# Performance work log

Measured on AMD Instinct MI355X. Metric: run time of the kernel, lower is better.

## Reference

```python
import jax, jax.numpy as jnp
import numpy as np

N = 100000      # num nodes
E = 1600000     # num edges
B = 256         # num graphs in batch
D_IN = 128
H = 256
BN_EPS = 1e-5


def setup_inputs() -> dict:
    key = jax.random.key(0)
    ks = jax.random.split(key, 16)
    inp = {}
    inp["x"] = jax.random.normal(ks[0], (N, D_IN), jnp.float32)
    inp["edge_index"] = jax.random.randint(ks[1], (2, E), 0, N, jnp.int32)
    inp["edge_weight"] = jax.random.uniform(ks[2], (E,), jnp.float32)
    inp["batch"] = jnp.sort(jax.random.randint(ks[3], (N,), 0, B, jnp.int32))
    # GCN layer 1
    inp["W1"] = jax.random.normal(ks[4], (D_IN, H), jnp.float32) * 0.05
    inp["b1"] = jnp.zeros((H,), jnp.float32)
    inp["g1"] = jnp.ones((H,), jnp.float32)
    inp["be1"] = jnp.zeros((H,), jnp.float32)
    inp["rm1"] = jnp.zeros((H,), jnp.float32)
    inp["rv1"] = jnp.ones((H,), jnp.float32)
    # GCN layer 2
    inp["W2"] = jax.random.normal(ks[5], (H, H), jnp.float32) * 0.05
    inp["b2"] = jnp.zeros((H,), jnp.float32)
    inp["g2"] = jnp.ones((H,), jnp.float32)
    inp["be2"] = jnp.zeros((H,), jnp.float32)
    inp["rm2"] = jnp.zeros((H,), jnp.float32)
    inp["rv2"] = jnp.ones((H,), jnp.float32)
    # classifier: Linear(256,256)+BN, Linear(256,128)+BN, Linear(128,2)
    inp["cW1"] = jax.random.normal(ks[6], (H, 256), jnp.float32) * 0.05
    inp["cb1"] = jnp.zeros((256,), jnp.float32)
    inp["cg1"] = jnp.ones((256,), jnp.float32)
    inp["cbe1"] = jnp.zeros((256,), jnp.float32)
    inp["crm1"] = jnp.zeros((256,), jnp.float32)
    inp["crv1"] = jnp.ones((256,), jnp.float32)
    inp["cW2"] = jax.random.normal(ks[7], (256, 128), jnp.float32) * 0.05
    inp["cb2"] = jnp.zeros((128,), jnp.float32)
    inp["cg2"] = jnp.ones((128,), jnp.float32)
    inp["cbe2"] = jnp.zeros((128,), jnp.float32)
    inp["crm2"] = jnp.zeros((128,), jnp.float32)
    inp["crv2"] = jnp.ones((128,), jnp.float32)
    inp["cW3"] = jax.random.normal(ks[8], (128, 2), jnp.float32) * 0.05
    inp["cb3"] = jnp.zeros((2,), jnp.float32)
    return inp


def _bn(x, g, b, rm, rv):
    # eval-mode BatchNorm1d with running stats
    return (x - rm) * jax.lax.rsqrt(rv + BN_EPS) * g + b


def _gcn_conv(x, W, b, src, dst, ew):
    # PyG GCNConv: add self-loops (weight 1), symmetric normalization
    deg = jax.ops.segment_sum(ew, dst, num_segments=N) + 1.0  # incl. self loop
    dinv = jnp.where(deg > 0, jax.lax.rsqrt(deg), 0.0)        # [N]
    h = x @ W                                                  # [N, out]
    norm = dinv[src] * ew * dinv[dst]                          # [E]
    agg = jax.ops.segment_sum(h[src] * norm[:, None], dst, num_segments=N)
    agg = agg + h * (dinv * dinv)[:, None]                     # self-loop term
    return agg + b


def _forward(x, edge_index, edge_weight, batch,
             W1, b1, g1, be1, rm1, rv1,
             W2, b2, g2, be2, rm2, rv2,
             cW1, cb1, cg1, cbe1, crm1, crv1,
             cW2, cb2, cg2, cbe2, crm2, crv2,
             cW3, cb3):
    src, dst = edge_index[0], edge_index[1]
    # layer 0 (no residual: i == 0)
    h = jax.nn.relu(_bn(_gcn_conv(x, W1, b1, src, dst, edge_weight), g1, be1, rm1, rv1))
    res = h
    # layer 1 (residual: dims match, i > 0); dropout = identity (eval)
    h = jax.nn.relu(_bn(_gcn_conv(h, W2, b2, src, dst, edge_weight), g2, be2, rm2, rv2))
    h = h + res
    # global mean pool per graph
    cnt = jax.ops.segment_sum(jnp.ones((N,), x.dtype), batch, num_segments=B)
    emb = jax.ops.segment_sum(h, batch, num_segments=B) / jnp.maximum(cnt, 1.0)[:, None]
    # classifier MLP
    z = jax.nn.relu(_bn(emb @ cW1 + cb1, cg1, cbe1, crm1, crv1))
    z = jax.nn.relu(_bn(z @ cW2 + cb2, cg2, cbe2, crm2, crv2))
    logits = z @ cW3 + cb3
    return logits, emb


def reference(x, edge_index, edge_weight, batch,
              W1, b1, g1, be1, rm1, rv1,
              W2, b2, g2, be2, rm2, rv2,
              cW1, cb1, cg1, cbe1, crm1, crv1,
              cW2, cb2, cg2, cbe2, crm2, crv2,
              cW3, cb3):
    return _forward(x, edge_index, edge_weight, batch,
                    W1, b1, g1, be1, rm1, rv1,
                    W2, b2, g2, be2, rm2, rv2,
                    cW1, cb1, cg1, cbe1, crm1, crv1,
                    cW2, cb2, cg2, cbe2, crm2, crv2,
                    cW3, cb3)
```

## Files before the change

kernel.cpp:

```cpp
#include <hip/hip_runtime.h>
#include <stdint.h>

#define NN 100000
#define NE 1600000
#define NB 256
#define DIN 128
#define HH 256
#define BN_EPS 1e-5f

typedef unsigned short bf16_t;
typedef __attribute__((ext_vector_type(8))) short short8;
typedef __attribute__((ext_vector_type(4))) short short4v;
typedef __attribute__((ext_vector_type(4))) float f32x4;
typedef __attribute__((ext_vector_type(2))) float f32x2;

struct __align__(8) EPair { int c; float v; };

#define DEG_MASK ((1ULL << 40) - 1ULL)
#define DEG_ONE  (1ULL << 40)
#define FXS 1048576.0f

__device__ __forceinline__ float bf2f(unsigned short u) {
    union { unsigned int i; float f; } v;
    v.i = ((unsigned int)u) << 16;
    return v.f;
}
__device__ __forceinline__ bf16_t f2bf(float f) {
    union { float f; unsigned int i; } v;
    v.f = f;
    unsigned int x = v.i;
    return (bf16_t)((x + 0x7fffu + ((x >> 16) & 1u)) >> 16);
}
__device__ __forceinline__ float ldp(const void* b, int i, int f) {
    return f ? ((const float*)b)[i] : bf2f(((const unsigned short*)b)[i]);
}
__device__ __forceinline__ int dflag_from(const void* rv) {
    return ((((const unsigned int*)rv)[0] & 0xffffu) == 0u) ? 1 : 0;
}

__device__ __forceinline__ void fmadd_row8p(f32x2* acc2, uint2 w, float v) {
#if defined(__HIP_DEVICE_COMPILE__)
    f32x2 vv = {v, v};
    acc2[0] += __builtin_amdgcn_cvt_pk_f32_fp8((int)w.x, false) * vv;
    acc2[1] += __builtin_amdgcn_cvt_pk_f32_fp8((int)w.x, true)  * vv;
    acc2[2] += __builtin_amdgcn_cvt_pk_f32_fp8((int)w.y, false) * vv;
    acc2[3] += __builtin_amdgcn_cvt_pk_f32_fp8((int)w.y, true)  * vv;
#else
    (void)acc2; (void)w; (void)v;
#endif
}
__device__ __forceinline__ unsigned char enc_fp8(float v) {
#if defined(__HIP_DEVICE_COMPILE__)
    int pk = __builtin_amdgcn_cvt_pk_fp8_f32(v, v, 0, false);
    return (unsigned char)(pk & 0xff);
#else
    (void)v; return 0;
#endif
}
__device__ __forceinline__ unsigned int pack4_fp8(float a, float b, float c, float d) {
#if defined(__HIP_DEVICE_COMPILE__)
    int w = __builtin_amdgcn_cvt_pk_fp8_f32(a, b, 0, false);
    w = __builtin_amdgcn_cvt_pk_fp8_f32(c, d, w, true);
    return (unsigned int)w;
#else
    (void)a; (void)b; (void)c; (void)d; return 0;
#endif
}

__device__ __forceinline__ void pack_one(const void* __restrict__ W, bf16_t* __restrict__ P,
                                         int S, int idx, int f) {
    int lane = idx & 63;
    int ts = idx >> 6;
    int s = ts % S;
    int t = ts / S;
    int q = lane >> 4, m = lane & 15;
    int colbase = t * 16 + m;
    int krow = 32 * s + 8 * q;
#pragma unroll
    for (int j = 0; j < 8; j++) P[idx * 8 + j] = f2bf(ldp(W, (krow + j) * 256 + colbase, f));
}

__global__ __launch_bounds__(256) void prep_kernel(const void* __restrict__ x, unsigned int* __restrict__ xc8,
                                                   const void* __restrict__ ew,
                                                   const int* __restrict__ dst,
                                                   const int* __restrict__ batch,
                                                   unsigned long long* __restrict__ cd8,
                                                   unsigned char* __restrict__ occ,
                                                   int* __restrict__ gcount,
                                                   const void* __restrict__ W1, bf16_t* __restrict__ P1,
                                                   const void* __restrict__ W2, bf16_t* __restrict__ P2,
                                                   const void* __restrict__ rv) {
    int i = blockIdx.x * blockDim.x + threadIdx.x;
    int stride = gridDim.x * blockDim.x;
    int shard = blockIdx.x & 7;
    int f = dflag_from(rv);
    if (i < 12288) {
        if (i < 4096) pack_one(W1, P1, 4, i, f);
        else          pack_one(W2, P2, 8, i - 4096, f);
    }
    if (f) {
        const float4* xs = (const float4*)x;
        for (int j = i; j < NN * DIN / 4; j += stride) {
            float4 w = xs[j];
            xc8[j] = pack4_fp8(w.x, w.y, w.z, w.w);
        }
    } else {
        const uint2* xs = (const uint2*)x;
        for (int j = i; j < NN * DIN / 4; j += stride) {
            uint2 w = xs[j];
            xc8[j] = pack4_fp8(bf2f((unsigned short)(w.x & 0xffffu)), bf2f((unsigned short)(w.x >> 16)),
                               bf2f((unsigned short)(w.y & 0xffffu)), bf2f((unsigned short)(w.y >> 16)));
        }
    }
    for (int j = i; j < NE; j += stride) {
        float w = ldp(ew, j, f);
        int d = dst[j];
        unsigned long long wfx = (unsigned long long)(unsigned int)(w * FXS + 0.5f);
        unsigned long long old = atomicAdd(&cd8[(size_t)shard * NN + d], DEG_ONE | wfx);
        occ[j] = (unsigned char)(old >> 40);
    }
    int lane = threadIdx.x & 63;
    for (int j = i; j < NN; j += stride) {
        int b = batch[j];
        bool boundary = (lane == 0) || (j == 0) || (batch[j - 1] != b);
        unsigned long long bmask = __ballot(boundary);
        bool islast = (lane == 63) || (j + 1 >= NN) || (batch[j + 1] != b);
        if (islast) {
            unsigned long long below = bmask & ((lane == 63) ? ~0ull : ((1ull << (lane + 1)) - 1ull));
            int first = 63 - __builtin_clzll(below);
            atomicAdd(&gcount[b], lane - first + 1);
        }
    }
}

#define SCAN_NB ((NN + 1023) / 1024)

__global__ __launch_bounds__(1024) void scanA(const unsigned long long* __restrict__ cd8,
                                              int* __restrict__ rowptr,
                                              float* __restrict__ dinv,
                                              int* __restrict__ bsum) {
    __shared__ int wsum[16];
    int tid = threadIdx.x, lane = tid & 63, wid = tid >> 6;
    int i = blockIdx.x * 1024 + tid;
    int v = 0;
    if (i < NN) {
        float wf = 0.f;
#pragma unroll
        for (int k = 0; k < 8; k++) {
            unsigned long long cv = cd8[(size_t)k * NN + i];
            v += (int)(cv >> 40);
            wf += (float)(cv & DEG_MASK);
        }
        dinv[i] = rsqrtf(wf * (1.0f / FXS) + 1.0f);
    }
    int sc = v;
#pragma unroll
    for (int off = 1; off < 64; off <<= 1) {
        int t = __shfl_up(sc, off, 64);
        if (lane >= off) sc += t;
    }
    if (lane == 63) wsum[wid] = sc;
    __syncthreads();
    if (wid == 0 && lane < 16) {
        int ws = wsum[lane];
        int scw = ws;
#pragma unroll
        for (int off = 1; off < 16; off <<= 1) {
            int t = __shfl_up(scw, off, 64);
            if (lane >= off) scw += t;
        }
        if (lane == 15) bsum[blockIdx.x] = scw;
        wsum[lane] = scw - ws;
    }
    __syncthreads();
    if (i < NN) rowptr[i] = wsum[wid] + sc - v;
}

__global__ __launch_bounds__(64) void scanB(int* __restrict__ bsum, int* __restrict__ rowptr,
                                            const int* __restrict__ gcount, int* __restrict__ gptr) {
    int lane = threadIdx.x;
    {
        int i0 = lane * 2;
        int v0 = (i0 < SCAN_NB) ? bsum[i0] : 0;
        int v1 = (i0 + 1 < SCAN_NB) ? bsum[i0 + 1] : 0;
        int tsum = v0 + v1;
        int sc = tsum;
#pragma unroll
        for (int off = 1; off < 64; off <<= 1) {
            int t = __shfl_up(sc, off, 64);
            if (lane >= off) sc += t;
        }
        int excl = sc - tsum;
        if (i0 < SCAN_NB) bsum[i0] = excl;
        if (i0 + 1 < SCAN_NB) bsum[i0 + 1] = excl + v0;
        if (lane == 63) rowptr[NN] = sc;
    }
    {
        int i0 = lane * 4;
        int v0 = gcount[i0], v1 = gcount[i0 + 1], v2 = gcount[i0 + 2], v3 = gcount[i0 + 3];
        int tsum = v0 + v1 + v2 + v3;
        int sc = tsum;
#pragma unroll
        for (int off = 1; off < 64; off <<= 1) {
            int t = __shfl_up(sc, off, 64);
            if (lane >= off) sc += t;
        }
        int excl = sc - tsum;
        gptr[i0] = excl;
        gptr[i0 + 1] = excl + v0;
        gptr[i0 + 2] = excl + v0 + v1;
        gptr[i0 + 3] = excl + v0 + v1 + v2;
        if (lane == 63) gptr[256] = sc;
    }
}

__global__ __launch_bounds__(1024) void scanC(int* __restrict__ rowptr, const int* __restrict__ bsum,
                                              const unsigned long long* __restrict__ cd8,
                                              int* __restrict__ offs) {
    int i = blockIdx.x * 1024 + threadIdx.x;
    if (i < NN) {
        int rp = rowptr[i] + bsum[blockIdx.x];
        rowptr[i] = rp;
        int cum = rp;
#pragma unroll
        for (int k = 0; k < 8; k++) {
            offs[(size_t)k * NN + i] = cum;
            cum += (int)(cd8[(size_t)k * NN + i] >> 40);
        }
    }
}

__global__ __launch_bounds__(256) void scatter_kernel(const int* __restrict__ src,
                                                      const int* __restrict__ dst,
                                                      const void* __restrict__ ew,
                                                      const float* __restrict__ dinv,
                                                      const int* __restrict__ offs,
                                                      const unsigned char* __restrict__ occ,
                                                      EPair* __restrict__ ep,
                                                      const void* __restrict__ rv) {
    int i = blockIdx.x * blockDim.x + threadIdx.x;
    int f = dflag_from(rv);
    int shard = blockIdx.x & 7;
    if (i < NE) {
        int s = src[i], d = dst[i];
        float nv = dinv[s] * ldp(ew, i, f) * dinv[d];
        int pos = offs[(size_t)shard * NN + d] + occ[i];
        EPair pr;
        pr.c = s;
        pr.v = nv;
        ep[pos] = pr;
    }
}

template <int K, bool WRITE_OUT, bool ACCUM>
__global__ __launch_bounds__(256, 6) void fused_layer(
        const void* __restrict__ Xv,
        const bf16_t* __restrict__ P,
        const int* __restrict__ rowptr,
        const EPair* __restrict__ ep,
        const float* __restrict__ dinv,
        const int* __restrict__ batch,
        const void* __restrict__ bias,
        const void* __restrict__ gam,
        const void* __restrict__ bet,
        const void* __restrict__ rmean,
        const void* __restrict__ rvar,
        void* __restrict__ outbuf,
        float* __restrict__ partial,
        float* __restrict__ partial2,
        float* __restrict__ embf) {
    constexpr int S = K / 32;
    constexpr int ROWELL = K + 8;
    constexpr int LPR = K / 8;
    constexpr int EDG = 64 / LPR;
    constexpr int UN = 8;
    constexpr int BE = EDG * UN;
    __shared__ __align__(16) bf16_t T[16 * ROWELL];
    const char* Xb = (const char*)Xv;
    int fl = dflag_from(rvar);
    int widx = threadIdx.x >> 6;
    int lane = threadIdx.x & 63;
    int h = lane / LPR;
    int l = lane % LPR;
    int f0 = l * 8;
    int rowbase = blockIdx.x * 16;

    int rp = rowptr[rowbase + (lane < 17 ? lane : 16)];
    float dvv = dinv[rowbase + (lane < 16 ? lane : 15)];

    int j0 = widx * 4;
    EPair win = ep[__shfl(rp, j0) + lane];
    for (int j = 0; j < 4; j++) {
        int r = j0 + j;
        int e0 = __shfl(rp, r);
        int e1 = __shfl(rp, r + 1);
        int n = e1 - e0;
        float di = __shfl(dvv, r);
        int node = rowbase + r;
        EPair nxtwin = ep[e1 + lane];
        f32x2 acc2[4];
#pragma unroll
        for (int c = 0; c < 4; c++) acc2[c] = (f32x2){0.f, 0.f};
        EPair cw = win;
        uint2 wself = *(const uint2*)(Xb + (size_t)node * K + l * 8);
        if (n <= 2 * BE) {
            uint2 wregA[UN], wregB[UN];
            float vregA[UN], vregB[UN];
#pragma unroll
            for (int u = 0; u < UN; u++) {
                int idx = EDG * u + h;
                bool ok = idx < n;
                int sl = ok ? idx : 0;
                int c = __shfl(cw.c, sl);
                float v = __shfl(cw.v, sl);
                wregA[u] = *(const uint2*)(Xb + (size_t)(ok ? c : node) * K + l * 8);
                vregA[u] = ok ? v : 0.f;
            }
#pragma unroll
            for (int u = 0; u < UN; u++) {
                int idx = BE + EDG * u + h;
                bool ok = idx < n;
                int sl = ok ? idx : 0;
                int c = __shfl(cw.c, sl);
                float v = __shfl(cw.v, sl);
                wregB[u] = *(const uint2*)(Xb + (size_t)(ok ? c : node) * K + l * 8);
                vregB[u] = ok ? v : 0.f;
            }
#pragma unroll
            for (int u = 0; u < UN; u++) fmadd_row8p(acc2, wregA[u], vregA[u]);
#pragma unroll
            for (int u = 0; u < UN; u++) fmadd_row8p(acc2, wregB[u], vregB[u]);
        } else {
            int base = 0;
            while (base < n) {
                int winend = n - base;
                if (winend > 64) winend = 64;
                for (int s0 = 0; s0 < winend; s0 += BE) {
                    uint2 wreg[UN];
                    float vreg[UN];
#pragma unroll
                    for (int u = 0; u < UN; u++) {
                        int idx = s0 + EDG * u + h;
                        bool ok = idx < winend;
                        int sl = ok ? idx : 0;
                        int c = __shfl(cw.c, sl);
                        float v = __shfl(cw.v, sl);
                        wreg[u] = *(const uint2*)(Xb + (size_t)(ok ? c : node) * K + l * 8);
                        vreg[u] = ok ? v : 0.f;
                    }
#pragma unroll
                    for (int u = 0; u < UN; u++) fmadd_row8p(acc2, wreg[u], vreg[u]);
                }
                base += winend;
                if (base < n) cw = ep[e0 + base + lane];
            }
        }
        fmadd_row8p(acc2, wself, (h == 0) ? di * di : 0.f);
        float acc[8];
#pragma unroll
        for (int c = 0; c < 4; c++) { acc[2 * c] = acc2[c][0]; acc[2 * c + 1] = acc2[c][1]; }
#pragma unroll
        for (int d = LPR; d < 64; d <<= 1) {
#pragma unroll
            for (int c = 0; c < 8; c++) acc[c] += __shfl_xor(acc[c], d);
        }
        if (h == 0) {
            short8 o;
#pragma unroll
            for (int c = 0; c < 8; c++) o[c] = (short)f2bf(acc[c]);
            *(short8*)&T[r * ROWELL + f0] = o;
        }
        win = nxtwin;
    }
    __syncthreads();

    int m = lane & 15, q = lane >> 4;
    f32x4 acc16[4];
#pragma unroll
    for (int tt = 0; tt < 4; tt++) acc16[tt] = (f32x4){0.f, 0.f, 0.f, 0.f};
#pragma unroll
    for (int s = 0; s < S; s++) {
        short8 af = *(const short8*)&T[m * ROWELL + 32 * s + 8 * q];
#pragma unroll
        for (int tt = 0; tt < 4; tt++) {
            int t = j0 + tt;
            short8 bfr = *(const short8*)(P + ((size_t)(t * S + s) * 64 + lane) * 8);
            acc16[tt] = __builtin_amdgcn_mfma_f32_16x16x32_bf16(af, bfr, acc16[tt], 0, 0, 0);
        }
    }
    if (WRITE_OUT) __syncthreads();
    unsigned char* T8 = (unsigned char*)T;

    int g0 = batch[rowbase];
    int g15 = batch[rowbase + 15];
    int rg[4];
#pragma unroll
    for (int r = 0; r < 4; r++) rg[r] = batch[rowbase + q * 4 + r];
#pragma unroll
    for (int tt = 0; tt < 4; tt++) {
        int col = (j0 + tt) * 16 + m;
        float a = rsqrtf(ldp(rvar, col, fl) + BN_EPS) * ldp(gam, col, fl);
        float bc = (ldp(bias, col, fl) - ldp(rmean, col, fl)) * a + ldp(bet, col, fl);
        float cs0 = 0.f, cs1 = 0.f;
#pragma unroll
        for (int r = 0; r < 4; r++) {
            int row = q * 4 + r;
            float v = fmaxf(acc16[tt][r] * a + bc, 0.f);
            if (WRITE_OUT) T8[row * 256 + col] = enc_fp8(v);
            if (rg[r] == g0) cs0 += v;
            else if (rg[r] == g15) cs1 += v;
            else atomicAdd(&embf[(size_t)rg[r] * 256 + col], v);
        }
        cs0 += __shfl_xor(cs0, 16, 64);
        cs0 += __shfl_xor(cs0, 32, 64);
        cs1 += __shfl_xor(cs1, 16, 64);
        cs1 += __shfl_xor(cs1, 32, 64);
        if (q == 0) {
            size_t pidx = (size_t)blockIdx.x * 256 + col;
            partial[pidx]  = (ACCUM ? partial[pidx]  : 0.f) + cs0;
            partial2[pidx] = (ACCUM ? partial2[pidx] : 0.f) + cs1;
        }
    }
    if (WRITE_OUT) {
        __syncthreads();
        int tid = threadIdx.x;
        uint4 wv = *(const uint4*)&T8[tid * 16];
        *(uint4*)((char*)outbuf + (size_t)rowbase * 256 + tid * 16) = wv;
    }
}

__global__ __launch_bounds__(256) void classifier_kernel(const float* __restrict__ partial,
                                                         const float* __restrict__ partial2,
                                                         const int* __restrict__ gptr,
                                                         const float* __restrict__ embf,
                                                         const void* cW1, const void* cb1,
                                                         const void* cg1, const void* cbe1,
                                                         const void* crm1, const void* crv1,
                                                         const void* cW2, const void* cb2,
                                                         const void* cg2, const void* cbe2,
                                                         const void* crm2, const void* crv2,
                                                         const void* cW3, const void* cb3,
                                                         void* __restrict__ d_out) {
    int g = blockIdx.x, tid = threadIdx.x;
    int fl = dflag_from(crv1);
    __shared__ float se[256];
    __shared__ float z1[256];
    __shared__ float z2[128];
    int s = gptr[g], e = gptr[g + 1];
    float acc = embf[g * 256 + tid];
    int blo = (s + 15) >> 4, bhi = (e + 15) >> 4;
    for (int b = blo; b < bhi; b++) acc += partial[(size_t)b * 256 + tid];
    int bs = s >> 4;
    if ((s & 15) && (16 * bs + 15) < e) acc += partial2[(size_t)bs * 256 + tid];
    float mval = acc / fmaxf((float)(e - s), 1.f);
    se[tid] = mval;
    if (fl) ((float*)d_out)[512 + g * 256 + tid] = mval;
    else    ((bf16_t*)d_out)[512 + g * 256 + tid] = f2bf(mval);
    __syncthreads();
    {
        float sm = 0.f;
#pragma unroll 8
        for (int k = 0; k < 256; k++) sm += se[k] * ldp(cW1, k * 256 + tid, fl);
        sm += ldp(cb1, tid, fl);
        sm = (sm - ldp(crm1, tid, fl)) * rsqrtf(ldp(crv1, tid, fl) + BN_EPS) * ldp(cg1, tid, fl) + ldp(cbe1, tid, fl);
        z1[tid] = fmaxf(sm, 0.f);
    }
    __syncthreads();
    if (tid < 128) {
        float sm = 0.f;
#pragma unroll 8
        for (int k = 0; k < 256; k++) sm += z1[k] * ldp(cW2, k * 128 + tid, fl);
        sm += ldp(cb2, tid, fl);
        sm = (sm - ldp(crm2, tid, fl)) * rsqrtf(ldp(crv2, tid, fl) + BN_EPS) * ldp(cg2, tid, fl) + ldp(cbe2, tid, fl);
        z2[tid] = fmaxf(sm, 0.f);
    }
    __syncthreads();
    if (tid < 2) {
        float sm = 0.f;
        for (int k = 0; k < 128; k++) sm += z2[k] * ldp(cW3, k * 2 + tid, fl);
        sm += ldp(cb3, tid, fl);
        if (fl) ((float*)d_out)[g * 2 + tid] = sm;
        else    ((bf16_t*)d_out)[g * 2 + tid] = f2bf(sm);
    }
}

extern "C" void kernel_launch(void* const* d_in, const int* in_sizes, int n_in,
                              void* d_out, int out_size, void* d_ws, size_t ws_size,
                              hipStream_t stream) {
    const void* x    = d_in[0];
    const int*  eidx = (const int*)d_in[1];
    const void* ew   = d_in[2];
    const int*  batch= (const int*)d_in[3];
    const void* W1   = d_in[4];
    const void* b1   = d_in[5];
    const void* g1   = d_in[6];
    const void* be1  = d_in[7];
    const void* rm1  = d_in[8];
    const void* rv1  = d_in[9];
    const void* W2   = d_in[10];
    const void* b2   = d_in[11];
    const void* g2   = d_in[12];
    const void* be2  = d_in[13];
    const void* rm2  = d_in[14];
    const void* rv2  = d_in[15];
    const void* cW1  = d_in[16];
    const void* cb1  = d_in[17];
    const void* cg1  = d_in[18];
    const void* cbe1 = d_in[19];
    const void* crm1 = d_in[20];
    const void* crv1 = d_in[21];
    const void* cW2  = d_in[22];
    const void* cb2  = d_in[23];
    const void* cg2  = d_in[24];
    const void* cbe2 = d_in[25];
    const void* crm2 = d_in[26];
    const void* crv2 = d_in[27];
    const void* cW3  = d_in[28];
    const void* cb3  = d_in[29];

    const int* src = eidx;
    const int* dst = eidx + NE;

    char* p = (char*)d_ws;
    auto alloc = [&](size_t bytes) -> void* {
        void* r = (void*)p;
        p += (bytes + 255) & ~(size_t)255;
        return r;
    };
    unsigned long long* cd8 = (unsigned long long*)alloc((size_t)8 * NN * 8);
    int*    gcount = (int*)alloc((size_t)NB * 4);
    float*  embf   = (float*)alloc((size_t)NB * 256 * 4);
    size_t zspan = (char*)p - (char*)cd8;
    int*    rowptr = (int*)alloc((size_t)(NN + 1) * 4);
    float*  dinv   = (float*)alloc((size_t)NN * 4);
    int*    bsum   = (int*)alloc((size_t)SCAN_NB * 4);
    int*    gptr   = (int*)alloc((size_t)(NB + 1) * 4);
    int*    offs   = (int*)alloc((size_t)8 * NN * 4);
    unsigned char* occ = (unsigned char*)alloc((size_t)NE);
    float*  partial = (float*)alloc((size_t)(NN / 16) * 256 * 4);
    float*  partial2= (float*)alloc((size_t)(NN / 16) * 256 * 4);
    EPair*  ep     = (EPair*)alloc((size_t)(NE + 64) * 8);
    unsigned int* xc8 = (unsigned int*)alloc((size_t)NN * DIN);
    bf16_t* pW1    = (bf16_t*)alloc((size_t)DIN * 256 * 2);
    bf16_t* pW2    = (bf16_t*)alloc((size_t)256 * 256 * 2);
    void*   hl     = alloc((size_t)NN * 256);

    (void)hipMemsetAsync(cd8, 0, zspan, stream);

    prep_kernel<<<2048, 256, 0, stream>>>(x, xc8, ew, dst, batch, cd8, occ, gcount,
                                          W1, pW1, W2, pW2, rv1);
    scanA<<<SCAN_NB, 1024, 0, stream>>>(cd8, rowptr, dinv, bsum);
    scanB<<<1, 64, 0, stream>>>(bsum, rowptr, gcount, gptr);
    scanC<<<SCAN_NB, 1024, 0, stream>>>(rowptr, bsum, cd8, offs);
    scatter_kernel<<<NE / 256, 256, 0, stream>>>(src, dst, ew, dinv, offs, occ, ep, rv1);

    int blocks = NN / 16;
    fused_layer<128, true, false><<<blocks, 256, 0, stream>>>(
        xc8, pW1, rowptr, ep, dinv, batch, b1, g1, be1, rm1, rv1, hl, partial, partial2, embf);
    fused_layer<256, false, true><<<blocks, 256, 0, stream>>>(
        hl, pW2, rowptr, ep, dinv, batch, b2, g2, be2, rm2, rv2, nullptr, partial, partial2, embf);

    classifier_kernel<<<NB, 256, 0, stream>>>(partial, partial2, gptr, embf,
                                              cW1, cb1, cg1, cbe1, crm1, crv1,
                                              cW2, cb2, cg2, cbe2, crm2, crv2,
                                              cW3, cb3, d_out);
}
```

Before: 527.0 us.

## Merge three scan kernels into one with grid barrier; vectorize edge scatter

Replaces the three-kernel prefix scan (block scan, single-block scan, fixup) with one kernel. The last-arriving block computes the block prefixes and graph pointers, and the other blocks spin on a flag, which removes two launches and the re-read of the per-shard counts. The edge scatter now handles four edges per thread with vector loads of src, dst and occupancy bytes. The shuffle-index select in the aggregation loop is also dropped. The spin barrier relies on all blocks being co-resident, which is a deadlock risk if they are not.

Result: no change. 531.3 us (+0.8%).

```diff
diff --git a/kernel.cpp b/kernel.cpp
--- a/kernel.cpp
+++ b/kernel.cpp
@@ -135,23 +135,34 @@
 
 #define SCAN_NB ((NN + 1023) / 1024)
 
-__global__ __launch_bounds__(1024) void scanA(const unsigned long long* __restrict__ cd8,
-                                              int* __restrict__ rowptr,
-                                              float* __restrict__ dinv,
-                                              int* __restrict__ bsum) {
+__global__ __launch_bounds__(1024) void scan_all(const unsigned long long* __restrict__ cd8,
+                                                 const int* __restrict__ gcount,
+                                                 int* __restrict__ rowptr,
+                                                 float* __restrict__ dinv,
+                                                 int* __restrict__ offs,
+                                                 int* __restrict__ gptr,
+                                                 int* __restrict__ ctrl,
+                                                 int* __restrict__ partials,
+                                                 int* __restrict__ prefix) {
     __shared__ int wsum[16];
+    __shared__ int s_off;
     int tid = threadIdx.x, lane = tid & 63, wid = tid >> 6;
-    int i = blockIdx.x * 1024 + tid;
+    int b = blockIdx.x;
+    int i = b * 1024 + tid;
     int v = 0;
+    int shardcnt[8];
+    float wf = 0.f;
     if (i < NN) {
-        float wf = 0.f;
 #pragma unroll
         for (int k = 0; k < 8; k++) {
             unsigned long long cv = cd8[(size_t)k * NN + i];
-            v += (int)(cv >> 40);
+            shardcnt[k] = (int)(cv >> 40);
+            v += shardcnt[k];
             wf += (float)(cv & DEG_MASK);
         }
-        dinv[i] = rsqrtf(wf * (1.0f / FXS) + 1.0f);
+    } else {
+#pragma unroll
+        for (int k = 0; k < 8; k++) shardcnt[k] = 0;
     }
     int sc = v;
 #pragma unroll
@@ -169,63 +180,45 @@
             int t = __shfl_up(scw, off, 64);
             if (lane >= off) scw += t;
         }
-        if (lane == 15) bsum[blockIdx.x] = scw;
+        if (lane == 15 && tid == 15) {}
         wsum[lane] = scw - ws;
-    }
-    __syncthreads();
-    if (i < NN) rowptr[i] = wsum[wid] + sc - v;
-}
-
-__global__ __launch_bounds__(64) void scanB(int* __restrict__ bsum, int* __restrict__ rowptr,
-                                            const int* __restrict__ gcount, int* __restrict__ gptr) {
-    int lane = threadIdx.x;
-    {
-        int i0 = lane * 2;
-        int v0 = (i0 < SCAN_NB) ? bsum[i0] : 0;
-        int v1 = (i0 + 1 < SCAN_NB) ? bsum[i0 + 1] : 0;
-        int tsum = v0 + v1;
-        int sc = tsum;
-#pragma unroll
-        for (int off = 1; off < 64; off <<= 1) {
-            int t = __shfl_up(sc, off, 64);
-            if (lane >= off) sc += t;
-        }
-        int excl = sc - tsum;
-        if (i0 < SCAN_NB) bsum[i0] = excl;
-        if (i0 + 1 < SCAN_NB) bsum[i0 + 1] = excl + v0;
-        if (lane == 63) rowptr[NN] = sc;
-    }
-    {
-        int i0 = lane * 4;
-        int v0 = gcount[i0], v1 = gcount[i0 + 1], v2 = gcount[i0 + 2], v3 = gcount[i0 + 3];
-        int tsum = v0 + v1 + v2 + v3;
-        int sc = tsum;
-#pragma unroll
-        for (int off = 1; off < 64; off <<= 1) {
-            int t = __shfl_up(sc, off, 64);
-            if (lane >= off) sc += t;
-        }
-        int excl = sc - tsum;
-        gptr[i0] = excl;
-        gptr[i0 + 1] = excl + v0;
-        gptr[i0 + 2] = excl + v0 + v1;
-        gptr[i0 + 3] = excl + v0 + v1 + v2;
-        if (lane == 63) gptr[256] = sc;
-    }
-}
-
-__global__ __launch_bounds__(1024) void scanC(int* __restrict__ rowptr, const int* __restrict__ bsum,
-                                              const unsigned long long* __restrict__ cd8,
-                                              int* __restrict__ offs) {
-    int i = blockIdx.x * 1024 + threadIdx.x;
+        if (lane == 15) partials[b] = scw;
+    }
+    __syncthreads();
+    if (tid == 0) {
+        __threadfence();
+        int old = atomicAdd(&ctrl[0], 1);
+        if (old == SCAN_NB - 1) {
+            __threadfence();
+            int run = 0;
+            for (int p = 0; p < SCAN_NB; p++) {
+                prefix[p] = run;
+                run += partials[p];
+            }
+            rowptr[NN] = run;
+            int g = 0;
+            for (int p = 0; p < NB; p++) {
+                gptr[p] = g;
+                g += gcount[p];
+            }
+            gptr[NB] = g;
+            __threadfence();
+            atomicExch(&ctrl[1], 1);
+        }
+        while (atomicAdd(&ctrl[1], 0) == 0) {}
+        __threadfence();
+        s_off = prefix[b];
+    }
+    __syncthreads();
     if (i < NN) {
-        int rp = rowptr[i] + bsum[blockIdx.x];
-        rowptr[i] = rp;
-        int cum = rp;
+        int base = s_off + wsum[wid] + (sc - v);
+        rowptr[i] = base;
+        dinv[i] = rsqrtf(wf * (1.0f / FXS) + 1.0f);
+        int cum = base;
 #pragma unroll
         for (int k = 0; k < 8; k++) {
             offs[(size_t)k * NN + i] = cum;
-            cum += (int)(cd8[(size_t)k * NN + i] >> 40);
+            cum += shardcnt[k];
         }
     }
 }
@@ -238,15 +231,22 @@
                                                       const unsigned char* __restrict__ occ,
                                                       EPair* __restrict__ ep,
                                                       const void* __restrict__ rv) {
-    int i = blockIdx.x * blockDim.x + threadIdx.x;
+    int t = blockIdx.x * blockDim.x + threadIdx.x;
+    if (t >= NE / 4) return;
     int f = dflag_from(rv);
-    int shard = blockIdx.x & 7;
-    if (i < NE) {
-        int s = src[i], d = dst[i];
-        float nv = dinv[s] * ldp(ew, i, f) * dinv[d];
-        int pos = offs[(size_t)shard * NN + d] + occ[i];
+    int base = t * 4;
+    int shard = (base >> 8) & 7;
+    uint4 s4 = ((const uint4*)src)[t];
+    uint4 d4 = ((const uint4*)dst)[t];
+    uint oc4 = ((const unsigned int*)occ)[t];
+    int ss[4] = {(int)s4.x, (int)s4.y, (int)s4.z, (int)s4.w};
+    int dd[4] = {(int)d4.x, (int)d4.y, (int)d4.z, (int)d4.w};
+#pragma unroll
+    for (int k = 0; k < 4; k++) {
+        float nv = dinv[ss[k]] * ldp(ew, base + k, f) * dinv[dd[k]];
+        int pos = offs[(size_t)shard * NN + dd[k]] + (int)((oc4 >> (8 * k)) & 0xffu);
         EPair pr;
-        pr.c = s;
+        pr.c = ss[k];
         pr.v = nv;
         ep[pos] = pr;
     }
@@ -310,9 +310,8 @@
             for (int u = 0; u < UN; u++) {
                 int idx = EDG * u + h;
                 bool ok = idx < n;
-                int sl = ok ? idx : 0;
-                int c = __shfl(cw.c, sl);
-                float v = __shfl(cw.v, sl);
+                int c = __shfl(cw.c, idx);
+                float v = __shfl(cw.v, idx);
                 wregA[u] = *(const uint2*)(Xb + (size_t)(ok ? c : node) * K + l * 8);
                 vregA[u] = ok ? v : 0.f;
             }
@@ -320,9 +319,8 @@
             for (int u = 0; u < UN; u++) {
                 int idx = BE + EDG * u + h;
                 bool ok = idx < n;
-                int sl = ok ? idx : 0;
-                int c = __shfl(cw.c, sl);
-                float v = __shfl(cw.v, sl);
+                int c = __shfl(cw.c, idx);
+                float v = __shfl(cw.v, idx);
                 wregB[u] = *(const uint2*)(Xb + (size_t)(ok ? c : node) * K + l * 8);
                 vregB[u] = ok ? v : 0.f;
             }
@@ -342,9 +340,8 @@
                     for (int u = 0; u < UN; u++) {
                         int idx = s0 + EDG * u + h;
                         bool ok = idx < winend;
-                        int sl = ok ? idx : 0;
-                        int c = __shfl(cw.c, sl);
-                        float v = __shfl(cw.v, sl);
+                        int c = __shfl(cw.c, idx);
+                        float v = __shfl(cw.v, idx);
                         wreg[u] = *(const uint2*)(Xb + (size_t)(ok ? c : node) * K + l * 8);
                         vreg[u] = ok ? v : 0.f;
                     }
@@ -530,10 +527,12 @@
     unsigned long long* cd8 = (unsigned long long*)alloc((size_t)8 * NN * 8);
     int*    gcount = (int*)alloc((size_t)NB * 4);
     float*  embf   = (float*)alloc((size_t)NB * 256 * 4);
+    int*    ctrl   = (int*)alloc(256);
     size_t zspan = (char*)p - (char*)cd8;
     int*    rowptr = (int*)alloc((size_t)(NN + 1) * 4);
     float*  dinv   = (float*)alloc((size_t)NN * 4);
-    int*    bsum   = (int*)alloc((size_t)SCAN_NB * 4);
+    int*    partials = (int*)alloc((size_t)SCAN_NB * 4);
+    int*    prefix   = (int*)alloc((size_t)SCAN_NB * 4);
     int*    gptr   = (int*)alloc((size_t)(NB + 1) * 4);
     int*    offs   = (int*)alloc((size_t)8 * NN * 4);
     unsigned char* occ = (unsigned char*)alloc((size_t)NE);
@@ -549,10 +548,9 @@
 
     prep_kernel<<<2048, 256, 0, stream>>>(x, xc8, ew, dst, batch, cd8, occ, gcount,
                                           W1, pW1, W2, pW2, rv1);
-    scanA<<<SCAN_NB, 1024, 0, stream>>>(cd8, rowptr, dinv, bsum);
-    scanB<<<1, 64, 0, stream>>>(bsum, rowptr, gcount, gptr);
-    scanC<<<SCAN_NB, 1024, 0, stream>>>(rowptr, bsum, cd8, offs);
-    scatter_kernel<<<NE / 256, 256, 0, stream>>>(src, dst, ew, dinv, offs, occ, ep, rv1);
+    scan_all<<<SCAN_NB, 1024, 0, stream>>>(cd8, gcount, rowptr, dinv, offs, gptr,
+                                           ctrl, partials, prefix);
+    scatter_kernel<<<(NE / 4 + 255) / 256, 256, 0, stream>>>(src, dst, ew, dinv, offs, occ, ep, rv1);
 
     int blocks = NN / 16;
     fused_layer<128, true, false><<<blocks, 256, 0, stream>>>(
```
